# Performance work log

Measured on AMD Instinct MI355X. Metric: run time of the kernel, lower is better.

The kernel has to match this reference:

```python
import jax, jax.numpy as jnp
import numpy as np

T, B, NMUL = 730, 1000, 8
NEARZERO = 1e-5
LENF = 15
A_LO, A_HI = 0.1, 1.0
B_LO, B_HI = 50.0, 500.0
C_LO, C_HI = 0.0, 1.0
D_LO, D_HI = 0.01, 0.9
RA_LO, RA_HI = 0.0, 2.9
RB_LO, RB_HI = 0.0, 6.5
S_INIT, G_INIT = 50.0, 10.0


def setup_inputs() -> dict:
    key = jax.random.key(0)
    k1, k2 = jax.random.split(key)
    # forcing: prcp in [0,10) mm/day, pet in [0,5) mm/day
    x = jax.random.uniform(k1, (T, B, 2), dtype=jnp.float32) * jnp.array([10.0, 5.0], dtype=jnp.float32)
    # NN-produced raw params in [0,1): 4*NMUL physical + 2 routing
    raw_phy_static = jax.random.uniform(k2, (B, 4 * NMUL + 2), dtype=jnp.float32)
    return {"x": x, "raw_phy_static": raw_phy_static}


def _descale(p, lo, hi):
    return p * (hi - lo) + lo


def _uh_gamma(rout_a, rout_b):
    # gamma-distribution unit hydrograph, (B,) params -> (B, LENF) kernel
    aa = jax.nn.relu(rout_a)[:, None] + 0.1      # shape parameter
    theta = jax.nn.relu(rout_b)[:, None] + 0.5   # scale parameter
    t = jnp.arange(0.5, LENF, 1.0, dtype=jnp.float32)[None, :]  # midpoints 0.5..14.5
    logw = (aa - 1.0) * jnp.log(t) - t / theta - jax.scipy.special.gammaln(aa) - aa * jnp.log(theta)
    w = jnp.exp(logw)
    return w / w.sum(1, keepdims=True)


def _uh_conv(q, UH):
    # causal per-basin convolution: y[b,t] = sum_k q[b,t-k]*UH[b,k]; q (B,T), UH (B,LENF)
    n = q.shape[1]
    conv1 = lambda qb, wb: jnp.convolve(qb, wb, mode='full')[:n]
    return jax.vmap(conv1)(q, UH)


def reference(x, raw_phy_static):
    phy = raw_phy_static[:, :4 * NMUL].reshape(B, 4, NMUL)  # (B,4,NMUL)
    a = _descale(phy[:, 0], A_LO, A_HI)
    b = _descale(phy[:, 1], B_LO, B_HI)
    c = _descale(phy[:, 2], C_LO, C_HI)
    d = _descale(phy[:, 3], D_LO, D_HI)
    rout_a = _descale(raw_phy_static[:, 4 * NMUL], RA_LO, RA_HI)  # (B,)
    rout_b = _descale(raw_phy_static[:, 4 * NMUL + 1], RB_LO, RB_HI)

    ones_mul = jnp.ones((1, 1, NMUL), dtype=x.dtype)
    P = x[:, :, 0:1] * ones_mul    # (T,B,NMUL)
    PET = x[:, :, 1:2] * ones_mul  # (T,B,NMUL)

    S0 = jnp.full((B, NMUL), S_INIT, dtype=x.dtype)
    G0 = jnp.full((B, NMUL), G_INIT, dtype=x.dtype)

    def step(carry, inp):
        S, G = carry
        p, pet = inp
        W = p + S                                   # available water
        term = (W + b) / (2.0 * a)
        Y = term - jnp.sqrt(jnp.maximum(term * term - W * b / a, NEARZERO))  # ET opportunity
        S_new = Y * jnp.exp(-pet / b)               # soil storage
        AET = Y - S_new                             # actual ET
        avail = W - Y                               # water available for runoff/recharge
        Qsurf = (1.0 - c) * avail                   # direct runoff
        G_new = (G + c * avail) / (1.0 + d)         # groundwater storage
        Qgw = d * G_new                             # baseflow
        Qsim = Qsurf + Qgw
        return (S_new, G_new), (Qsim, Qsurf, Qgw, AET, S_new, G_new, W, Y)

    (_, _), (Qsim, Qsurf, Qgw, AET, Sout, Gout, Wout, Yout) = jax.lax.scan(step, (S0, G0), (P, PET))

    UH = _uh_gamma(rout_a, rout_b)                  # (B,LENF)
    Qs = _uh_conv(Qsim.mean(-1).T, UH).T[..., None]        # routed streamflow (T,B,1)
    Qsurf_r = _uh_conv(Qsurf.mean(-1).T, UH).T[..., None]  # routed surface runoff
    Qgw_r = _uh_conv(Qgw.mean(-1).T, UH).T[..., None]      # routed groundwater flow

    out = jnp.concatenate([
        Qs, Qsurf_r, Qgw_r,
        AET.mean(-1, keepdims=True),
        Sout.mean(-1, keepdims=True),
        Gout.mean(-1, keepdims=True),
    ], axis=-1)  # (T,B,6)
    return out
```

## Files before the change

kernel.cpp:

```cpp
#include <hip/hip_runtime.h>
#include <math.h>

#define T_STEPS 730
#define NB      1000
#define LENF    15
#define NEARZ   1e-5f
#define SGW     8000
#define TT      32
#define BBLK    32

#define STEPA(CURV)                                                            \
  {                                                                            \
    float pcp = (CURV).x, pet = (CURV).y;                                      \
    float W     = pcp + S;                                                     \
    float term  = fmaf(W, inv2a, pb2a);                                        \
    float disc  = fmaf(term, term, -(W * boa));                                \
    float r     = __builtin_amdgcn_sqrtf(fmaxf(disc, NEARZ));                  \
    float Y     = term - r;                                                    \
    float e     = __builtin_amdgcn_exp2f(pet * nbl);                           \
    float Sn    = Y * e;                                                       \
    float avail = W - Y;                                                       \
    float Gn    = fmaf(pc, avail, G) * i1d;                                    \
    S = Sn; G = Gn;                                                            \
    *psg = make_float2(Sn, Gn);                                                \
    psg += SGW;                                                                \
  }

#define PREFETCH(BUF, CI)                                                      \
  _Pragma("unroll")                                                            \
  for (int j = 0; j < 8; ++j) {                                                \
      int tt = (CI) * 8 + j;                                                   \
      tt = tt < T_STEPS ? tt : (T_STEPS - 1);                                  \
      BUF[j] = xf[tt * NB + b];                                                \
  }                                                                            \
  __builtin_amdgcn_sched_barrier(0);

__global__ __launch_bounds__(64, 1) void scan_state(const float* __restrict__ x,
                                                    const float* __restrict__ raw,
                                                    float2* __restrict__ sg) {
    const int L   = threadIdx.x;
    const int gid = blockIdx.x * 64 + L;
    const int b   = gid >> 3;
    const int m   = gid & 7;

    const float* rp = raw + b * 34;
    float pa = rp[0 * 8 + m] * 0.9f + 0.1f;
    float pb = rp[1 * 8 + m] * 450.0f + 50.0f;
    float pc = rp[2 * 8 + m];
    float pd = rp[3 * 8 + m] * 0.89f + 0.01f;

    float inv2a = 1.0f / (2.0f * pa);
    float pb2a  = pb * inv2a;
    float boa   = pb / pa;
    float nbl   = -1.4426950408889634f / pb;
    float i1d   = 1.0f / (1.0f + pd);

    float S = 50.0f, G = 10.0f;
    float2* psg = sg + gid;

    const float2* __restrict__ xf = (const float2*)x;

    float2 A[8], Bb[8], Cc[8];
    PREFETCH(A, 0)
    PREFETCH(Bb, 1)

    for (int g = 0; g < 15; ++g) {
        const int c0 = 6 * g;
        PREFETCH(Cc, c0 + 2)
#pragma unroll
        for (int j = 0; j < 8; ++j) STEPA(A[j])
        PREFETCH(A, c0 + 3)
#pragma unroll
        for (int j = 0; j < 8; ++j) STEPA(Bb[j])
        PREFETCH(Bb, c0 + 4)
#pragma unroll
        for (int j = 0; j < 8; ++j) STEPA(Cc[j])
        PREFETCH(Cc, c0 + 5)
#pragma unroll
        for (int j = 0; j < 8; ++j) STEPA(A[j])
        PREFETCH(A, c0 + 6)
#pragma unroll
        for (int j = 0; j < 8; ++j) STEPA(Bb[j])
        PREFETCH(Bb, c0 + 7)
#pragma unroll
        for (int j = 0; j < 8; ++j) STEPA(Cc[j])
    }
#pragma unroll
    for (int j = 0; j < 8; ++j) STEPA(A[j])
    STEPA(Bb[0])
    STEPA(Bb[1])
}

template <int CTRL>
__device__ __forceinline__ float dpp_mov(float x) {
    int xi = __builtin_bit_cast(int, x);
    int r  = __builtin_amdgcn_update_dpp(0, xi, CTRL, 0xF, 0xF, true);
    return __builtin_bit_cast(float, r);
}
__device__ __forceinline__ float sum8(float v) {
    v += dpp_mov<0xB1>(v);
    v += dpp_mov<0x4E>(v);
    v += dpp_mov<0x141>(v);
    return v;
}

__global__ __launch_bounds__(256) void finalize(const float* __restrict__ x,
                                                const float* __restrict__ raw,
                                                const float2* __restrict__ sg,
                                                float* __restrict__ out) {
    __shared__ float qsh[TT + 14][BBLK + 1];
    __shared__ float qgh[TT + 14][BBLK + 1];

    const int tid   = threadIdx.x;
    const int lb    = tid >> 3;
    const int m     = tid & 7;
    const int tbase = blockIdx.x * TT;
    const int b0    = blockIdx.y * BBLK;
    const int b     = b0 + lb;
    const bool bval = b < NB;
    const int bc    = bval ? b : (NB - 1);
    const int lane  = bc * 8 + m;

    const float* rp = raw + bc * 34;
    float pbm = rp[8 + m] * 450.0f + 50.0f;
    float e2s = 1.4426950408889634f / pbm;
    float omc = 1.0f - rp[16 + m];
    float dm  = rp[24 + m] * 0.89f + 0.01f;

    const float2* __restrict__ xf = (const float2*)x;

    float Sprev = 50.0f;
    int tt0  = tbase - 14;
    int ttc0 = tt0 < 0 ? 0 : tt0;
    float2 sgv = sg[(size_t)ttc0 * SGW + lane];
    float2 pv  = xf[ttc0 * NB + bc];

    for (int r = 0; r < TT + 14; ++r) {
        const int tt = tbase + r - 14;
        int ttn = tt + 1;
        ttn = ttn < 0 ? 0 : (ttn >= T_STEPS ? T_STEPS - 1 : ttn);
        float2 sgn = sg[(size_t)ttn * SGW + lane];
        float2 pvn = xf[ttn * NB + bc];

        const bool tval = (tt >= 0) && (tt < T_STEPS);
        float qs = 0.0f, qg = 0.0f, aet = 0.0f, sX = 0.0f, gX = 0.0f;
        if (tval) {
            float sp    = (tt == 0) ? 50.0f : Sprev;
            float y     = sgv.x * __builtin_amdgcn_exp2f(pv.y * e2s);
            float avail = (pv.x + sp) - y;
            qs  = omc * avail;
            qg  = dm * sgv.y;
            aet = y - sgv.x;
            sX  = sgv.x;
            gX  = sgv.y;
        }
        qs = sum8(qs);
        qg = sum8(qg);
        if (m == 0) { qsh[r][lb] = qs; qgh[r][lb] = qg; }
        if (r >= 14 && tval) {
            float a_s = sum8(aet);
            float s_s = sum8(sX);
            float g_s = sum8(gX);
            if (bval && m < 3) {
                float v = (m == 0) ? a_s : ((m == 1) ? s_s : g_s);
                out[((size_t)tt * NB + b) * 6 + 3 + m] = v * 0.125f;
            }
        }
        Sprev = sgv.x;
        sgv = sgn; pv = pvn;
    }
    __syncthreads();

    const int bl2 = tid & 31;
    const int tl0 = tid >> 5;
    const int b2  = b0 + bl2;
    if (b2 >= NB) return;

    const float* rp2 = raw + b2 * 34;
    float ra = rp2[32] * 2.9f;
    float rb = rp2[33] * 6.5f;
    float aa = fmaxf(ra, 0.0f) + 0.1f;
    float th = fmaxf(rb, 0.0f) + 0.5f;
    float inv_th = 1.0f / th;
    float am1 = aa - 1.0f;
    float w[LENF];
    float sw = 0.0f;
#pragma unroll
    for (int k = 0; k < LENF; ++k) {
        float tk = (float)k + 0.5f;
        w[k] = __expf(am1 * __logf(tk) - tk * inv_th);
        sw += w[k];
    }
    float invs = 0.125f / sw;
#pragma unroll
    for (int k = 0; k < LENF; ++k) w[k] *= invs;

#pragma unroll
    for (int it = 0; it < 4; ++it) {
        int tl = tl0 + it * 8;
        int t  = tbase + tl;
        if (t < T_STEPS) {
            float ys = 0.0f, yg = 0.0f;
#pragma unroll
            for (int k = 0; k < LENF; ++k) {
                ys = fmaf(qsh[tl + 14 - k][bl2], w[k], ys);
                yg = fmaf(qgh[tl + 14 - k][bl2], w[k], yg);
            }
            float* o = out + ((size_t)t * NB + b2) * 6;
            o[0] = ys + yg;
            o[1] = ys;
            o[2] = yg;
        }
    }
}

#define STEPF(CURV)                                                            \
  {                                                                            \
    float pcp = (CURV).x, pet = (CURV).y;                                      \
    float W     = pcp + S;                                                     \
    float term  = fmaf(W, inv2a, pb2a);                                        \
    float disc  = fmaf(term, term, -(W * boa));                                \
    float r     = __builtin_amdgcn_sqrtf(fmaxf(disc, NEARZ));                  \
    float Y     = term - r;                                                    \
    float e     = __builtin_amdgcn_exp2f(pet * ninvbl2);                       \
    float Sn    = Y * e;                                                       \
    float AET   = Y - Sn;                                                      \
    float avail = W - Y;                                                       \
    float Qs    = omc * avail;                                                 \
    float Gn    = fmaf(pc, avail, G) * inv1pd;                                 \
    float Qg    = pd * Gn;                                                     \
    S = Sn; G = Gn;                                                            \
    float qs_s = sum8(Qs);                                                     \
    float qg_s = sum8(Qg);                                                     \
    float ae_s = sum8(AET);                                                    \
    float s_s  = sum8(Sn);                                                     \
    float g_s  = sum8(Gn);                                                     \
    float v = qs_s;                                                            \
    v = (m == 1) ? qg_s : v;                                                   \
    v = (m == 2) ? ae_s : v;                                                   \
    v = (m == 3) ? s_s  : v;                                                   \
    v = (m >= 4) ? g_s  : v;                                                   \
    *optr = v * 0.125f;                                                        \
    optr += incr;                                                              \
  }

__global__ __launch_bounds__(64, 1) void scan_fb(const float* __restrict__ x,
                                                 const float* __restrict__ raw,
                                                 float* __restrict__ out,
                                                 float* __restrict__ qs_ws,
                                                 float* __restrict__ qg_ws,
                                                 float* __restrict__ dummy) {
    const int L  = threadIdx.x;
    const int lb = L >> 3;
    const int m  = L & 7;
    const int b  = blockIdx.x * 8 + lb;

    const float* rp = raw + b * 34;
    float pa = rp[0 * 8 + m] * 0.9f + 0.1f;
    float pb = rp[1 * 8 + m] * 450.0f + 50.0f;
    float pc = rp[2 * 8 + m];
    float pd = rp[3 * 8 + m] * 0.89f + 0.01f;
    float inv2a   = 1.0f / (2.0f * pa);
    float pb2a    = pb * inv2a;
    float boa     = pb / pa;
    float ninvbl2 = -1.4426950408889634f / pb;
    float omc     = 1.0f - pc;
    float inv1pd  = 1.0f / (1.0f + pd);

    float* optr;
    long long incr;
    if      (m == 0) { optr = qs_ws + b;                      incr = NB;     }
    else if (m == 1) { optr = qg_ws + b;                      incr = NB;     }
    else if (m <= 4) { optr = out + (long long)b * 6 + m + 1; incr = NB * 6; }
    else             { optr = dummy + (blockIdx.x * 64 + L);  incr = 0;      }

    float S = 50.0f, G = 10.0f;
    const float2* __restrict__ xf = (const float2*)x;

    float2 A[10], B[10], C[10];
#pragma unroll
    for (int j = 0; j < 10; ++j) A[j] = xf[j * NB + b];
#pragma unroll
    for (int j = 0; j < 10; ++j) B[j] = xf[(10 + j) * NB + b];

    for (int cg = 0; cg < 24; ++cg) {
        const int c0 = 3 * cg;
#pragma unroll
        for (int j = 0; j < 10; ++j) C[j] = xf[((c0 + 2) * 10 + j) * NB + b];
        __builtin_amdgcn_sched_barrier(0);
#pragma unroll
        for (int j = 0; j < 10; ++j) STEPF(A[j]);
#pragma unroll
        for (int j = 0; j < 10; ++j) A[j] = xf[((c0 + 3) * 10 + j) * NB + b];
        __builtin_amdgcn_sched_barrier(0);
#pragma unroll
        for (int j = 0; j < 10; ++j) STEPF(B[j]);
#pragma unroll
        for (int j = 0; j < 10; ++j) {
            int t = (c0 + 4) * 10 + j;
            t = t < T_STEPS ? t : (T_STEPS - 1);
            B[j] = xf[t * NB + b];
        }
        __builtin_amdgcn_sched_barrier(0);
#pragma unroll
        for (int j = 0; j < 10; ++j) STEPF(C[j]);
    }
#pragma unroll
    for (int j = 0; j < 10; ++j) STEPF(A[j]);
}

__global__ __launch_bounds__(256) void uh_fb(const float* __restrict__ raw,
                                             float* __restrict__ uh) {
    int b = blockIdx.x * 256 + threadIdx.x;
    if (b >= NB) return;
    float ra = raw[b * 34 + 32] * 2.9f;
    float rb = raw[b * 34 + 33] * 6.5f;
    float aa = fmaxf(ra, 0.0f) + 0.1f;
    float th = fmaxf(rb, 0.0f) + 0.5f;
    float inv_th = 1.0f / th;
    float am1 = aa - 1.0f;
    float w[LENF];
    float s = 0.0f;
#pragma unroll
    for (int k = 0; k < LENF; ++k) {
        float t = (float)k + 0.5f;
        w[k] = __expf(am1 * __logf(t) - t * inv_th);
        s += w[k];
    }
    float invs = 1.0f / s;
#pragma unroll
    for (int k = 0; k < LENF; ++k) uh[k * NB + b] = w[k] * invs;
}

__global__ __launch_bounds__(256) void conv_fb(const float* __restrict__ qs_ws,
                                               const float* __restrict__ qg_ws,
                                               const float* __restrict__ uh,
                                               float* __restrict__ out) {
    int b = blockIdx.x * 256 + threadIdx.x;
    int t = blockIdx.y;
    if (b >= NB) return;
    float ys = 0.0f, yg = 0.0f;
    int kmax = t < (LENF - 1) ? t : (LENF - 1);
    for (int k = 0; k <= kmax; ++k) {
        float w = uh[k * NB + b];
        ys = fmaf(qs_ws[(t - k) * NB + b], w, ys);
        yg = fmaf(qg_ws[(t - k) * NB + b], w, yg);
    }
    float* o = out + (t * NB + b) * 6;
    o[0] = ys + yg;
    o[1] = ys;
    o[2] = yg;
}

extern "C" void kernel_launch(void* const* d_in, const int* in_sizes, int n_in,
                              void* d_out, int out_size, void* d_ws, size_t ws_size,
                              hipStream_t stream) {
    const float* x   = (const float*)d_in[0];
    const float* raw = (const float*)d_in[1];
    float* out = (float*)d_out;

    const size_t need = (size_t)T_STEPS * SGW * sizeof(float2);
    if (ws_size >= need) {
        float2* sg = (float2*)d_ws;
        scan_state<<<dim3(SGW / 64), dim3(64),  0, stream>>>(x, raw, sg);
        finalize  <<<dim3((T_STEPS + TT - 1) / TT, (NB + BBLK - 1) / BBLK),
                     dim3(256), 0, stream>>>(x, raw, sg, out);
    } else {
        float* qs = (float*)d_ws;
        float* qg = qs + (size_t)T_STEPS * NB;
        float* uh = qg + (size_t)T_STEPS * NB;
        float* dm = uh + (size_t)LENF * NB;
        uh_fb  <<<dim3((NB + 255) / 256),          dim3(256), 0, stream>>>(raw, uh);
        scan_fb<<<dim3(NB / 8),                    dim3(64),  0, stream>>>(x, raw, out, qs, qg, dm);
        conv_fb<<<dim3((NB + 255) / 256, T_STEPS), dim3(256), 0, stream>>>(qs, qg, uh, out);
    }
}
```

Before: 123.2 us.

## Stage forcing into LDS for scan, deepen output-pass prefetch, enlarge time tile

The scan kernel now bulk-loads each block's whole forcing slice (8 basins by 730 steps) into shared memory with float4 loads up front, then reads its per-step inputs from LDS. This replaces the strided global loads that sat on the serial recurrence. The output kernel's time tile grows from 32 to 50 and its state and forcing loads are software-pipelined four steps ahead to hide global latency. In exchange the scan pays an upfront load-and-barrier phase and heavy register use for the staging buffer, and the larger tile means fewer blocks and more halo recompute per block.

```diff
diff --git a/kernel.cpp b/kernel.cpp
--- a/kernel.cpp
+++ b/kernel.cpp
@@ -6,7 +6,7 @@
 #define LENF    15
 #define NEARZ   1e-5f
 #define SGW     8000
-#define TT      32
+#define TT      50
 #define BBLK    32
 
 #define STEPA(CURV)                                                            \
@@ -29,19 +29,37 @@
 #define PREFETCH(BUF, CI)                                                      \
   _Pragma("unroll")                                                            \
   for (int j = 0; j < 8; ++j) {                                                \
-      int tt = (CI) * 8 + j;                                                   \
-      tt = tt < T_STEPS ? tt : (T_STEPS - 1);                                  \
-      BUF[j] = xf[tt * NB + b];                                                \
+      BUF[j] = xs[((CI) * 8 + j) * 8 + bl];                                    \
   }                                                                            \
   __builtin_amdgcn_sched_barrier(0);
 
 __global__ __launch_bounds__(64, 1) void scan_state(const float* __restrict__ x,
                                                     const float* __restrict__ raw,
                                                     float2* __restrict__ sg) {
+    __shared__ float4 xs4[2944];
+    const float2* xs = (const float2*)xs4;
+
     const int L   = threadIdx.x;
     const int gid = blockIdx.x * 64 + L;
     const int b   = gid >> 3;
     const int m   = gid & 7;
+    const int bl  = L >> 3;
+
+    {
+        float4 tmp[46];
+#pragma unroll
+        for (int ch = 0; ch < 46; ++ch) {
+            int idx = ch * 64 + L;
+            int row = idx >> 2;
+            row = row < T_STEPS ? row : (T_STEPS - 1);
+            tmp[ch] = *(const float4*)((const char*)x + (size_t)row * (NB * 8)
+                                       + (size_t)(blockIdx.x * 64)
+                                       + (size_t)(idx & 3) * 16);
+        }
+#pragma unroll
+        for (int ch = 0; ch < 46; ++ch) xs4[ch * 64 + L] = tmp[ch];
+    }
+    __syncthreads();
 
     const float* rp = raw + b * 34;
     float pa = rp[0 * 8 + m] * 0.9f + 0.1f;
@@ -57,8 +75,6 @@
 
     float S = 50.0f, G = 10.0f;
     float2* psg = sg + gid;
-
-    const float2* __restrict__ xf = (const float2*)x;
 
     float2 A[8], Bb[8], Cc[8];
     PREFETCH(A, 0)
@@ -129,45 +145,55 @@
 
     const float2* __restrict__ xf = (const float2*)x;
 
-    float Sprev = 50.0f;
-    int tt0  = tbase - 14;
-    int ttc0 = tt0 < 0 ? 0 : tt0;
-    float2 sgv = sg[(size_t)ttc0 * SGW + lane];
-    float2 pv  = xf[ttc0 * NB + bc];
-
-    for (int r = 0; r < TT + 14; ++r) {
-        const int tt = tbase + r - 14;
-        int ttn = tt + 1;
-        ttn = ttn < 0 ? 0 : (ttn >= T_STEPS ? T_STEPS - 1 : ttn);
-        float2 sgn = sg[(size_t)ttn * SGW + lane];
-        float2 pvn = xf[ttn * NB + bc];
-
-        const bool tval = (tt >= 0) && (tt < T_STEPS);
-        float qs = 0.0f, qg = 0.0f, aet = 0.0f, sX = 0.0f, gX = 0.0f;
-        if (tval) {
-            float sp    = (tt == 0) ? 50.0f : Sprev;
-            float y     = sgv.x * __builtin_amdgcn_exp2f(pv.y * e2s);
-            float avail = (pv.x + sp) - y;
-            qs  = omc * avail;
-            qg  = dm * sgv.y;
-            aet = y - sgv.x;
-            sX  = sgv.x;
-            gX  = sgv.y;
+    float2 sgb[4], pvb[4];
+#pragma unroll
+    for (int d = 0; d < 4; ++d) {
+        int tt = tbase + d - 14;
+        int tc = tt < 0 ? 0 : (tt >= T_STEPS ? T_STEPS - 1 : tt);
+        sgb[d] = sg[(size_t)tc * SGW + lane];
+        pvb[d] = xf[tc * NB + bc];
+    }
+    float Sprev = (tbase > 0) ? sg[(size_t)(tbase - 15) * SGW + lane].x : 50.0f;
+
+    for (int rr = 0; rr < TT + 14; rr += 4) {
+#pragma unroll
+        for (int d = 0; d < 4; ++d) {
+            const int r  = rr + d;
+            const int tt = tbase + r - 14;
+            float2 sgv = sgb[d];
+            float2 pv  = pvb[d];
+            {
+                int tn = tt + 4;
+                int tc = tn < 0 ? 0 : (tn >= T_STEPS ? T_STEPS - 1 : tn);
+                sgb[d] = sg[(size_t)tc * SGW + lane];
+                pvb[d] = xf[tc * NB + bc];
+            }
+            const bool tval = (tt >= 0) && (tt < T_STEPS);
+            float qs = 0.0f, qg = 0.0f, aet = 0.0f, sX = 0.0f, gX = 0.0f;
+            if (tval) {
+                float sp    = (tt == 0) ? 50.0f : Sprev;
+                float y     = sgv.x * __builtin_amdgcn_exp2f(pv.y * e2s);
+                float avail = (pv.x + sp) - y;
+                qs  = omc * avail;
+                qg  = dm * sgv.y;
+                aet = y - sgv.x;
+                sX  = sgv.x;
+                gX  = sgv.y;
+            }
+            qs = sum8(qs);
+            qg = sum8(qg);
+            if (m == 0) { qsh[r][lb] = qs; qgh[r][lb] = qg; }
+            if (r >= 14 && tval) {
+                float a_s = sum8(aet);
+                float s_s = sum8(sX);
+                float g_s = sum8(gX);
+                if (bval && m < 3) {
+                    float v = (m == 0) ? a_s : ((m == 1) ? s_s : g_s);
+                    out[((size_t)tt * NB + b) * 6 + 3 + m] = v * 0.125f;
+                }
+            }
+            Sprev = sgv.x;
         }
-        qs = sum8(qs);
-        qg = sum8(qg);
-        if (m == 0) { qsh[r][lb] = qs; qgh[r][lb] = qg; }
-        if (r >= 14 && tval) {
-            float a_s = sum8(aet);
-            float s_s = sum8(sX);
-            float g_s = sum8(gX);
-            if (bval && m < 3) {
-                float v = (m == 0) ? a_s : ((m == 1) ? s_s : g_s);
-                out[((size_t)tt * NB + b) * 6 + 3 + m] = v * 0.125f;
-            }
-        }
-        Sprev = sgv.x;
-        sgv = sgn; pv = pvn;
     }
     __syncthreads();
 
@@ -196,10 +222,10 @@
     for (int k = 0; k < LENF; ++k) w[k] *= invs;
 
 #pragma unroll
-    for (int it = 0; it < 4; ++it) {
+    for (int it = 0; it < 7; ++it) {
         int tl = tl0 + it * 8;
         int t  = tbase + tl;
-        if (t < T_STEPS) {
+        if (tl < TT && t < T_STEPS) {
             float ys = 0.0f, yg = 0.0f;
 #pragma unroll
             for (int k = 0; k < LENF; ++k) {
```

New measurement: 113.6 us. 1.08x faster.
